# Performance work log

Measured on AMD Instinct MI355X. Metric: run time of the kernel, lower is better.

## Reference

```python
import jax, jax.numpy as jnp
import numpy as np
from jax.ops import segment_sum

NEG_SLOPE = 0.01  # torch F.leaky_relu default

N_NODES = 100000
N_EDGES = 1600000
IN_FEAT = 67
HIDDEN = 256
N_CLASS = 18
N_GRAPHS = 256


def setup_inputs() -> dict:
    key = jax.random.key(0)
    ks = jax.random.split(key, 12)
    h = jax.random.normal(ks[0], (N_NODES, IN_FEAT), dtype=jnp.float32)
    src = jax.random.randint(ks[1], (N_EDGES,), 0, N_NODES, dtype=jnp.int32)
    dst = jax.random.randint(ks[2], (N_EDGES,), 0, N_NODES, dtype=jnp.int32)
    graph_ids = jnp.sort(jax.random.randint(ks[3], (N_NODES,), 0, N_GRAPHS, dtype=jnp.int32))
    s = 0.05
    W1_self = jax.random.normal(ks[4], (IN_FEAT, HIDDEN), dtype=jnp.float32) * s
    W1_neigh = jax.random.normal(ks[5], (IN_FEAT, HIDDEN), dtype=jnp.float32) * s
    b1 = jnp.zeros((HIDDEN,), dtype=jnp.float32)
    W2_self = jax.random.normal(ks[6], (HIDDEN, HIDDEN), dtype=jnp.float32) * s
    W2_neigh = jax.random.normal(ks[7], (HIDDEN, HIDDEN), dtype=jnp.float32) * s
    b2 = jnp.zeros((HIDDEN,), dtype=jnp.float32)
    Wfc = jax.random.normal(ks[8], (HIDDEN, N_CLASS), dtype=jnp.float32) * s
    bfc = jnp.zeros((N_CLASS,), dtype=jnp.float32)
    return {
        "h": h, "W1_self": W1_self, "W1_neigh": W1_neigh, "b1": b1,
        "W2_self": W2_self, "W2_neigh": W2_neigh, "b2": b2,
        "Wfc": Wfc, "bfc": bfc,
        "src": src, "dst": dst, "graph_ids": graph_ids, "num_graphs": N_GRAPHS,
    }


def _sage_mean(h, Wself, Wneigh, b, src, dst, n_nodes):
    # DGL SAGEConv(mean): h_neigh = mean over incoming neighbors; 0 if no neighbors
    agg = segment_sum(h[src], dst, num_segments=n_nodes)          # [N, D]
    deg = segment_sum(jnp.ones_like(dst, dtype=h.dtype), dst, num_segments=n_nodes)
    h_neigh = agg / jnp.maximum(deg, 1.0)[:, None]
    return h @ Wself + h_neigh @ Wneigh + b


def reference(h, W1_self, W1_neigh, b1, W2_self, W2_neigh, b2, Wfc, bfc,
              src, dst, graph_ids, num_graphs):
    n_nodes = h.shape[0]
    x = jax.nn.leaky_relu(_sage_mean(h, W1_self, W1_neigh, b1, src, dst, n_nodes), NEG_SLOPE)
    x = jax.nn.leaky_relu(_sage_mean(x, W2_self, W2_neigh, b2, src, dst, n_nodes), NEG_SLOPE)
    # dgl.mean_nodes: per-graph mean pooling over nodes
    gsum = segment_sum(x, graph_ids, num_segments=num_graphs)       # [G, D]
    gcnt = segment_sum(jnp.ones((n_nodes,), dtype=x.dtype), graph_ids, num_segments=num_graphs)
    hg = gsum / jnp.maximum(gcnt, 1.0)[:, None]
    return hg @ Wfc + bfc  # [G, n_classifier]
```

## Files before the change

kernel.cpp:

```cpp
#include <hip/hip_runtime.h>

#define WAVE 64
#define OW 256
#define LDA1 96
#define NCHUNK 64
#define PBITS 15
#define PBINS (1 << PBITS)
#define NPART 4

typedef short bf16x8 __attribute__((ext_vector_type(8)));
typedef float f32x4  __attribute__((ext_vector_type(4)));
typedef float f32x2  __attribute__((ext_vector_type(2)));

__device__ __forceinline__ unsigned short f2bf(float f) {
    unsigned int u = __float_as_uint(f);
    u = (u + 0x7FFF + ((u >> 16) & 1)) >> 16;
    return (unsigned short)u;
}
__device__ __forceinline__ float bf2f(unsigned short u) {
    return __uint_as_float(((unsigned int)u) << 16);
}
__device__ __forceinline__ float bflo(unsigned int u) { return __uint_as_float(u << 16); }
__device__ __forceinline__ float bfhi(unsigned int u) { return __uint_as_float(u & 0xFFFF0000u); }
__device__ __forceinline__ unsigned int packbf(float lo, float hi) {
    return (unsigned int)f2bf(lo) | ((unsigned int)f2bf(hi) << 16);
}
__device__ __forceinline__ float lrelu(float x) { return x > 0.0f ? x : 0.01f * x; }

__device__ __forceinline__ unsigned int pack4_f8(float v0, float v1, float v2, float v3) {
    int p = __builtin_amdgcn_cvt_pk_fp8_f32(v0, v1, 0, false);
    p = __builtin_amdgcn_cvt_pk_fp8_f32(v2, v3, p, true);
    return (unsigned int)p;
}
__device__ __forceinline__ unsigned char enc1_f8(float v) {
    return (unsigned char)(__builtin_amdgcn_cvt_pk_fp8_f32(v, 0.0f, 0, false) & 0xFF);
}
__device__ __forceinline__ void acc4_f8(float* a, unsigned int u) {
    f32x2 lo = __builtin_amdgcn_cvt_pk_f32_fp8(u, false);
    f32x2 hi = __builtin_amdgcn_cvt_pk_f32_fp8(u, true);
    a[0] += lo.x; a[1] += lo.y; a[2] += hi.x; a[3] += hi.y;
}


__device__ __forceinline__ void pack_b_body(const float* __restrict__ Ws,
                                            const float* __restrict__ Wn,
                                            unsigned short* __restrict__ Bb,
                                            int KHALF, int KT_HALF, int idx) {
    int e  = idx & 7;
    int l  = (idx >> 3) & 63;
    int nt = (idx >> 9) & 15;
    int kt = idx >> 13;
    int n  = nt * 16 + (l & 15);
    int kh = (kt < KT_HALF ? kt : kt - KT_HALF) * 32 + (l >> 4) * 8 + e;
    const float* W = (kt < KT_HALF) ? Ws : Wn;
    float v = (kh < KHALF) ? W[(size_t)kh * OW + n] : 0.0f;
    Bb[idx] = f2bf(v);
}

__global__ void prep_kernel(const float* __restrict__ h, unsigned int* __restrict__ hb,
                            unsigned int* __restrict__ hb8, int N, int K,
                            const float* __restrict__ W1s, const float* __restrict__ W1n,
                            unsigned short* __restrict__ Bb1,
                            const float* __restrict__ W2s, const float* __restrict__ W2n,
                            unsigned short* __restrict__ Bb2) {
    const int tid = blockIdx.x * blockDim.x + threadIdx.x;
    const int nth = gridDim.x * blockDim.x;

    const int tot_h = N * (LDA1 / 2);
    for (int i = tid; i < tot_h; i += nth) {
        int row = i / (LDA1 / 2);
        int c   = (i - row * (LDA1 / 2)) * 2;
        float v0 = (c     < K) ? h[(size_t)row * K + c]     : 0.0f;
        float v1 = (c + 1 < K) ? h[(size_t)row * K + c + 1] : 0.0f;
        hb[i] = packbf(v0, v1);
    }
    const int tot8 = N * (LDA1 / 4);
    for (int i = tid; i < tot8; i += nth) {
        int row = i / (LDA1 / 4);
        int c   = (i - row * (LDA1 / 4)) * 4;
        const float* hr = h + (size_t)row * K;
        float v0 = (c     < K) ? hr[c]     : 0.0f;
        float v1 = (c + 1 < K) ? hr[c + 1] : 0.0f;
        float v2 = (c + 2 < K) ? hr[c + 2] : 0.0f;
        float v3 = (c + 3 < K) ? hr[c + 3] : 0.0f;
        hb8[i] = pack4_f8(v0, v1, v2, v3);
    }
    for (int i = tid; i < 2 * 3 * 16 * 64 * 8; i += nth)
        pack_b_body(W1s, W1n, Bb1, K, 3, i);
    for (int i = tid; i < 2 * 8 * 16 * 64 * 8; i += nth)
        pack_b_body(W2s, W2n, Bb2, OW, 8, i);
}


__global__ __launch_bounds__(512) void hist_kernel(const int* __restrict__ dst, int E, int N,
                                                   unsigned short* __restrict__ hist,
                                                   unsigned short* __restrict__ rank_local) {
    __shared__ unsigned int lcnt[PBINS / 2];
    const int c    = blockIdx.x / NPART;
    const int p    = blockIdx.x - c * NPART;
    const int base = p << PBITS;
    const int nb   = (N - base < PBINS) ? (N - base) : PBINS;
    if (nb <= 0) return;
    const int che = (E + NCHUNK - 1) / NCHUNK;
    const int beg = c * che;
    const int end = (beg + che < E) ? (beg + che) : E;

    for (int i = threadIdx.x; i < PBINS / 2; i += 512) lcnt[i] = 0;
    __syncthreads();

    auto proc = [&](int d, int e) {
        d -= base;
        if ((unsigned)d < (unsigned)nb) {
            unsigned int sh  = (d & 1) * 16;
            unsigned int old = atomicAdd(&lcnt[d >> 1], 1u << sh);
            rank_local[e] = (unsigned short)((old >> sh) & 0xFFFFu);
        }
    };

    if (((beg | end) & 3) == 0) {
        const int4* dst4 = (const int4*)(dst + beg);
        const int n4 = (end - beg) >> 2;
        for (int i = threadIdx.x; i < n4; i += 512) {
            int4 d = dst4[i];
            int e = beg + 4 * i;
            proc(d.x, e + 0);
            proc(d.y, e + 1);
            proc(d.z, e + 2);
            proc(d.w, e + 3);
        }
    } else {
        for (int e = beg + (int)threadIdx.x; e < end; e += 512)
            proc(dst[e], e);
    }
    __syncthreads();

    unsigned short* hrow = hist + (size_t)c * N + base;
    for (int i = threadIdx.x; i < nb; i += 512) {
        unsigned int v = lcnt[i >> 1];
        hrow[i] = (unsigned short)((v >> ((i & 1) * 16)) & 0xFFFFu);
    }
}

__global__ void chunk_scan_kernel(unsigned short* __restrict__ hist, int* __restrict__ cnt,
                                  int N) {
    int bin = blockIdx.x * blockDim.x + threadIdx.x;
    if (bin >= N) return;
    int s = 0;
#pragma unroll 8
    for (int c = 0; c < NCHUNK; ++c) {
        size_t idx = (size_t)c * N + bin;
        int t = hist[idx];
        hist[idx] = (unsigned short)s;
        s += t;
    }
    cnt[bin] = s;
}

__global__ __launch_bounds__(1024) void scan_blocksum(const int* __restrict__ cnt,
                                                      int* __restrict__ bsum, int n) {
    __shared__ int s[1024];
    int i = blockIdx.x * 1024 + threadIdx.x;
    s[threadIdx.x] = (i < n) ? cnt[i] : 0;
    __syncthreads();
    for (int off = 512; off > 0; off >>= 1) {
        if (threadIdx.x < off) s[threadIdx.x] += s[threadIdx.x + off];
        __syncthreads();
    }
    if (threadIdx.x == 0) bsum[blockIdx.x] = s[0];
}

__global__ __launch_bounds__(128) void scan_offsets(int* __restrict__ bsum, int nb) {
    __shared__ int s[128];
    int v = (threadIdx.x < nb) ? bsum[threadIdx.x] : 0;
    s[threadIdx.x] = v;
    __syncthreads();
    for (int off = 1; off < 128; off <<= 1) {
        int t = (threadIdx.x >= off) ? s[threadIdx.x - off] : 0;
        __syncthreads();
        s[threadIdx.x] += t;
        __syncthreads();
    }
    if (threadIdx.x < nb) bsum[threadIdx.x] = s[threadIdx.x] - v;
}

__global__ __launch_bounds__(1024) void scan_write(const int* __restrict__ cnt,
                                                   const int* __restrict__ boff,
                                                   int* __restrict__ rowptr, int n) {
    __shared__ int s[1024];
    int i = blockIdx.x * 1024 + threadIdx.x;
    int v = (i < n) ? cnt[i] : 0;
    s[threadIdx.x] = v;
    __syncthreads();
    for (int off = 1; off < 1024; off <<= 1) {
        int t = (threadIdx.x >= off) ? s[threadIdx.x - off] : 0;
        __syncthreads();
        s[threadIdx.x] += t;
        __syncthreads();
    }
    if (i < n) rowptr[i + 1] = boff[blockIdx.x] + s[threadIdx.x];
    if (i == 0) rowptr[0] = 0;
}

__global__ void fill_kernel(const int* __restrict__ src, const int* __restrict__ dst,
                            const unsigned short* __restrict__ rank_local,
                            const int* __restrict__ rowptr,
                            const unsigned short* __restrict__ hist,
                            int* __restrict__ csr, int E, int N) {
    const int che = (E + NCHUNK - 1) / NCHUNK;
    const int tid = blockIdx.x * blockDim.x + threadIdx.x;
    const int nth = gridDim.x * blockDim.x;

    if ((che & 3) == 0) {
        const int e4 = E >> 2;
        const int4* dst4 = (const int4*)dst;
        const int4* src4 = (const int4*)src;
        const ushort4* r4 = (const ushort4*)rank_local;
        for (int i = tid; i < e4; i += nth) {
            int4 d = dst4[i];
            int4 s = src4[i];
            ushort4 r = r4[i];
            const unsigned short* hrow = hist + (size_t)(4 * i / che) * N;
            csr[rowptr[d.x] + (int)hrow[d.x] + (int)r.x] = s.x;
            csr[rowptr[d.y] + (int)hrow[d.y] + (int)r.y] = s.y;
            csr[rowptr[d.z] + (int)hrow[d.z] + (int)r.z] = s.z;
            csr[rowptr[d.w] + (int)hrow[d.w] + (int)r.w] = s.w;
        }
        for (int e = e4 * 4 + tid; e < E; e += nth) {
            int d = dst[e];
            csr[rowptr[d] + (int)hist[(size_t)(e / che) * N + d] + (int)rank_local[e]] = src[e];
        }
    } else {
        for (int e = tid; e < E; e += nth) {
            int d = dst[e];
            csr[rowptr[d] + (int)hist[(size_t)(e / che) * N + d] + (int)rank_local[e]] = src[e];
        }
    }
}


__global__ void gather_mean256_f8(const unsigned char* __restrict__ feat,
                                  const int* __restrict__ rowptr, const int* __restrict__ csr,
                                  unsigned int* __restrict__ aggm, int N) {
    const int lane = threadIdx.x & (WAVE - 1);
    const int grp  = lane >> 4;
    const int sub  = lane & 15;
    int wave = (blockIdx.x * blockDim.x + threadIdx.x) / WAVE;
    int nw   = (gridDim.x * blockDim.x) / WAVE;

    for (int v = wave; v < N; v += nw) {
        const int beg = rowptr[v], deg = rowptr[v + 1] - beg;
        float a[16];
#pragma unroll
        for (int i = 0; i < 16; ++i) a[i] = 0.0f;

        const int noct = deg >> 3;
        for (int i = 0; i < noct; ++i) {
            int e0 = csr[beg + 8 * i + grp];
            int e1 = csr[beg + 8 * i + 4 + grp];
            uint4 x0 = *(const uint4*)(feat + (size_t)e0 * 256 + sub * 16);
            uint4 x1 = *(const uint4*)(feat + (size_t)e1 * 256 + sub * 16);
            acc4_f8(a + 0,  x0.x); acc4_f8(a + 4,  x0.y);
            acc4_f8(a + 8,  x0.z); acc4_f8(a + 12, x0.w);
            acc4_f8(a + 0,  x1.x); acc4_f8(a + 4,  x1.y);
            acc4_f8(a + 8,  x1.z); acc4_f8(a + 12, x1.w);
        }
        for (int e = (noct << 3) + grp; e < deg; e += 4) {
            int s = csr[beg + e];
            uint4 x = *(const uint4*)(feat + (size_t)s * 256 + sub * 16);
            acc4_f8(a + 0,  x.x); acc4_f8(a + 4,  x.y);
            acc4_f8(a + 8,  x.z); acc4_f8(a + 12, x.w);
        }
#pragma unroll
        for (int i = 0; i < 16; ++i) {
            a[i] += __shfl_xor(a[i], 16);
            a[i] += __shfl_xor(a[i], 32);
        }
        if (grp == 0) {
            float inv = 1.0f / fmaxf((float)deg, 1.0f);
            unsigned int o[8];
#pragma unroll
            for (int i = 0; i < 8; ++i)
                o[i] = packbf(a[2 * i] * inv, a[2 * i + 1] * inv);
            unsigned int* dst0 = aggm + (size_t)v * 128 + sub * 8;
            *(uint4*)(dst0)     = make_uint4(o[0], o[1], o[2], o[3]);
            *(uint4*)(dst0 + 4) = make_uint4(o[4], o[5], o[6], o[7]);
        }
    }
}

__global__ void gather_mean_pad_f8(const unsigned char* __restrict__ feat,
                                   const int* __restrict__ rowptr, const int* __restrict__ csr,
                                   unsigned int* __restrict__ aggm, int N) {
    const int lane = threadIdx.x & (WAVE - 1);
    const int half = lane >> 5;
    const int sub  = lane & 31;
    const bool act = sub < 24;
    int wave = (blockIdx.x * blockDim.x + threadIdx.x) / WAVE;
    int nw   = (gridDim.x * blockDim.x) / WAVE;

    for (int v = wave; v < N; v += nw) {
        const int beg = rowptr[v], deg = rowptr[v + 1] - beg;
        const int npairs = deg >> 1;
        float a[4] = {0.f, 0.f, 0.f, 0.f};

        int p = 0;
        for (; p + 3 < npairs; p += 4) {
            int i0 = csr[beg + 2 * (p + 0) + half];
            int i1 = csr[beg + 2 * (p + 1) + half];
            int i2 = csr[beg + 2 * (p + 2) + half];
            int i3 = csr[beg + 2 * (p + 3) + half];
            if (act) {
                unsigned int x0 = *(const unsigned int*)(feat + (size_t)i0 * 96 + sub * 4);
                unsigned int x1 = *(const unsigned int*)(feat + (size_t)i1 * 96 + sub * 4);
                unsigned int x2 = *(const unsigned int*)(feat + (size_t)i2 * 96 + sub * 4);
                unsigned int x3 = *(const unsigned int*)(feat + (size_t)i3 * 96 + sub * 4);
                acc4_f8(a, x0); acc4_f8(a, x1); acc4_f8(a, x2); acc4_f8(a, x3);
            }
        }
        for (; p < npairs; ++p) {
            int i0 = csr[beg + 2 * p + half];
            if (act) {
                unsigned int x0 = *(const unsigned int*)(feat + (size_t)i0 * 96 + sub * 4);
                acc4_f8(a, x0);
            }
        }
        if ((deg & 1) && half == 0) {
            int i0 = csr[beg + deg - 1];
            if (act) {
                unsigned int x0 = *(const unsigned int*)(feat + (size_t)i0 * 96 + sub * 4);
                acc4_f8(a, x0);
            }
        }
#pragma unroll
        for (int i = 0; i < 4; ++i) a[i] += __shfl_xor(a[i], 32);

        if (half == 0 && act) {
            float inv = 1.0f / fmaxf((float)deg, 1.0f);
            uint2 o;
            o.x = packbf(a[0] * inv, a[1] * inv);
            o.y = packbf(a[2] * inv, a[3] * inv);
            *(uint2*)(aggm + (size_t)v * 48 + sub * 2) = o;
        }
    }
}

template<int KT_HALF, int CHUNK, bool F8OUT>
__global__ __launch_bounds__(256) void sage_mfma(
    const unsigned short* __restrict__ Hs, const unsigned short* __restrict__ Hn, int lda,
    const unsigned short* __restrict__ Bb, const float* __restrict__ bias,
    unsigned short* __restrict__ outb, unsigned char* __restrict__ out8, int M)
{
    constexpr int NT    = 2 * KT_HALF;
    constexpr int NCH   = NT / CHUNK;
    constexpr int CELEM = CHUNK * 16 * 64;
    constexpr int CPT   = CELEM / 256;
    __shared__ bf16x8 Bs[CELEM];

    const int t    = threadIdx.x;
    const int lane = t & 63, wid = t >> 6;
    const int wm   = wid >> 1, wn = wid & 1;
    const int brow = blockIdx.x * 64;
    const int lrow = lane & 15, kblk = lane >> 4;

    const int r0 = brow + wm * 32 + lrow;
    const int r1 = r0 + 16;
    const int r0c = (r0 < M) ? r0 : (M - 1);
    const int r1c = (r1 < M) ? r1 : (M - 1);

    f32x4 acc[2][8];
#pragma unroll
    for (int rt = 0; rt < 2; ++rt)
#pragma unroll
        for (int ct = 0; ct < 8; ++ct) acc[rt][ct] = (f32x4)0.0f;

    auto loadA = [&](int ch, bf16x8 (&a0)[CHUNK], bf16x8 (&a1)[CHUNK]) {
#pragma unroll
        for (int k = 0; k < CHUNK; ++k) {
            int kt = ch * CHUNK + k;
            bool self = kt < KT_HALF;
            int kh = (self ? kt : kt - KT_HALF) * 32 + kblk * 8;
            const unsigned short* srcp = self ? Hs : Hn;
            a0[k] = *(const bf16x8*)(srcp + (size_t)r0c * lda + kh);
            a1[k] = *(const bf16x8*)(srcp + (size_t)r1c * lda + kh);
        }
    };

    const bf16x8* gB = (const bf16x8*)Bb;
    bf16x8 tmpB[CPT];
    bf16x8 a0[CHUNK], a1[CHUNK];
#pragma unroll
    for (int i = 0; i < CPT; ++i) tmpB[i] = gB[i * 256 + t];
    loadA(0, a0, a1);

#pragma unroll
    for (int ch = 0; ch < NCH; ++ch) {
        __syncthreads();
#pragma unroll
        for (int i = 0; i < CPT; ++i) Bs[i * 256 + t] = tmpB[i];
        __syncthreads();

        bf16x8 nB[CPT], n0[CHUNK], n1[CHUNK];
        if (ch + 1 < NCH) {
            const bf16x8* g = gB + (size_t)(ch + 1) * CELEM;
#pragma unroll
            for (int i = 0; i < CPT; ++i) nB[i] = g[i * 256 + t];
            loadA(ch + 1, n0, n1);
        }

#pragma unroll
        for (int k = 0; k < CHUNK; ++k) {
            const bf16x8* bp = &Bs[(k * 16 + wn * 8) * 64 + lane];
#pragma unroll
            for (int ct = 0; ct < 8; ++ct) {
                bf16x8 b = bp[ct * 64];
                acc[0][ct] = __builtin_amdgcn_mfma_f32_16x16x32_bf16(a0[k], b, acc[0][ct], 0, 0, 0);
                acc[1][ct] = __builtin_amdgcn_mfma_f32_16x16x32_bf16(a1[k], b, acc[1][ct], 0, 0, 0);
            }
        }
        if (ch + 1 < NCH) {
#pragma unroll
            for (int i = 0; i < CPT; ++i) tmpB[i] = nB[i];
#pragma unroll
            for (int k = 0; k < CHUNK; ++k) { a0[k] = n0[k]; a1[k] = n1[k]; }
        }
    }

#pragma unroll
    for (int rt = 0; rt < 2; ++rt) {
        int rbase = brow + wm * 32 + rt * 16 + kblk * 4;
#pragma unroll
        for (int ct = 0; ct < 8; ++ct) {
            int col = wn * 128 + ct * 16 + lrow;
            float vb = bias[col];
#pragma unroll
            for (int j = 0; j < 4; ++j) {
                int row = rbase + j;
                if (row < M) {
                    float v = lrelu(acc[rt][ct][j] + vb);
                    outb[(size_t)row * OW + col] = f2bf(v);
                    if (F8OUT)
                        out8[(size_t)row * OW + col] = enc1_f8(v);
                }
            }
        }
    }
}


__global__ __launch_bounds__(256) void pool_fc_kernel(
    const unsigned short* __restrict__ x, const int* __restrict__ gid,
    const float* __restrict__ Wfc, const float* __restrict__ bfc,
    float* __restrict__ out, int N, int C)
{
    int g = blockIdx.x;
    int lo = 0, hi = N;
    while (lo < hi) { int m = (lo + hi) >> 1; if (gid[m] < g) lo = m + 1; else hi = m; }
    int beg = lo;
    hi = N;
    while (lo < hi) { int m = (lo + hi) >> 1; if (gid[m] <= g) lo = m + 1; else hi = m; }
    int end = lo;

    __shared__ float hg[OW];
    int c = threadIdx.x;
    float s0 = 0.f, s1 = 0.f, s2 = 0.f, s3 = 0.f;
    int r = beg;
    for (; r + 3 < end; r += 4) {
        s0 += bf2f(x[(size_t)(r + 0) * OW + c]);
        s1 += bf2f(x[(size_t)(r + 1) * OW + c]);
        s2 += bf2f(x[(size_t)(r + 2) * OW + c]);
        s3 += bf2f(x[(size_t)(r + 3) * OW + c]);
    }
    for (; r < end; ++r) s0 += bf2f(x[(size_t)r * OW + c]);
    float s = (s0 + s1) + (s2 + s3);
    float inv = (end > beg) ? 1.0f / (float)(end - beg) : 0.0f;
    hg[c] = s * inv;
    __syncthreads();

    if (c < C) {
        float a = bfc[c];
        for (int k = 0; k < OW; ++k)
            a = fmaf(hg[k], Wfc[(size_t)k * C + c], a);
        out[(size_t)g * C + c] = a;
    }
}

extern "C" void kernel_launch(void* const* d_in, const int* in_sizes, int n_in,
                              void* d_out, int out_size, void* d_ws, size_t ws_size,
                              hipStream_t stream) {
    const float* h   = (const float*)d_in[0];
    const float* W1s = (const float*)d_in[1];
    const float* W1n = (const float*)d_in[2];
    const float* b1  = (const float*)d_in[3];
    const float* W2s = (const float*)d_in[4];
    const float* W2n = (const float*)d_in[5];
    const float* b2  = (const float*)d_in[6];
    const float* Wfc = (const float*)d_in[7];
    const float* bfc = (const float*)d_in[8];
    const int*   src = (const int*)d_in[9];
    const int*   dst = (const int*)d_in[10];
    const int*   gid = (const int*)d_in[11];

    const int N  = in_sizes[11];
    const int E  = in_sizes[9];
    const int K1 = in_sizes[0] / N;
    const int NC = in_sizes[8];
    const int G  = out_size / NC;

    char* w = (char*)d_ws;
    auto alloc = [&](size_t bytes) { char* p = w; w += (bytes + 255) & ~(size_t)255; return p; };
    unsigned int*   hb     = (unsigned int*)alloc((size_t)N * (LDA1 / 2) * 4);
    unsigned int*   hb8    = (unsigned int*)alloc((size_t)N * LDA1);
    unsigned int*   agg1b  = (unsigned int*)alloc((size_t)N * (LDA1 / 2) * 4);
    unsigned short* x1b    = (unsigned short*)alloc((size_t)N * OW * 2);
    unsigned char*  x1f8   = (unsigned char*)alloc((size_t)N * OW);
    unsigned short* agg2b  = (unsigned short*)alloc((size_t)N * OW * 2);
    int*            rowptr = (int*)alloc((size_t)(N + 1) * 4);
    int*            cnt    = (int*)alloc((size_t)N * 4);
    int*            csr    = (int*)alloc((size_t)E * 4);
    unsigned short* rankl  = (unsigned short*)alloc((size_t)E * 2);
    unsigned short* hist   = (unsigned short*)alloc((size_t)NCHUNK * N * 2);
    int*            bsum   = (int*)alloc(1024 * 4);
    unsigned short* Bb1    = (unsigned short*)alloc((size_t)2 * 3 * 16 * 64 * 8 * 2);
    unsigned short* Bb2    = (unsigned short*)alloc((size_t)2 * 8 * 16 * 64 * 8 * 2);

    float* out = (float*)d_out;
    const int nb = (N + 1023) / 1024;

    hist_kernel<<<NCHUNK * NPART, 512, 0, stream>>>(dst, E, N, hist, rankl);
    chunk_scan_kernel<<<(N + 255) / 256, 256, 0, stream>>>(hist, cnt, N);
    scan_blocksum<<<nb, 1024, 0, stream>>>(cnt, bsum, N);
    scan_offsets<<<1, 128, 0, stream>>>(bsum, nb);
    scan_write<<<nb, 1024, 0, stream>>>(cnt, bsum, rowptr, N);
    fill_kernel<<<2048, 256, 0, stream>>>(src, dst, rankl, rowptr, hist, csr, E, N);

    prep_kernel<<<2048, 256, 0, stream>>>(h, hb, hb8, N, K1, W1s, W1n, Bb1, W2s, W2n, Bb2);

    const int gemm_grid = (N + 63) / 64;

    gather_mean_pad_f8<<<4096, 256, 0, stream>>>((const unsigned char*)hb8, rowptr, csr,
                                                 agg1b, N);
    sage_mfma<3, 2, true><<<gemm_grid, 256, 0, stream>>>((const unsigned short*)hb,
                                                         (const unsigned short*)agg1b, LDA1,
                                                         Bb1, b1, x1b, x1f8, N);

    gather_mean256_f8<<<4096, 256, 0, stream>>>(x1f8, rowptr, csr,
                                                (unsigned int*)agg2b, N);
    sage_mfma<8, 2, false><<<gemm_grid, 256, 0, stream>>>(x1b, agg2b, OW, Bb2, b2,
                                                          x1b, nullptr, N);

    pool_fc_kernel<<<G, 256, 0, stream>>>(x1b, gid, Wfc, bfc, out, N, NC);
}
```

Before: 355.1 us.

## Merge histogram with input prep kernel and fuse chunk scan with block sums

The histogram kernel and the feature/weight packing kernel become one launch, with separate block ranges running the two independent jobs concurrently. The per-bin chunk scan now also does the per-block reduction that the separate scan_blocksum kernel used to do. This removes two kernel launches and lets the latency-bound histogram overlap with the bandwidth-bound prep. The cost is that prep blocks now also reserve the histogram's 64KB of shared memory, which lowers occupancy, and the chunk scan runs at 1024 threads per block.

After: 357.6 us. About the same (+0.7%).

```diff
diff --git a/kernel.cpp b/kernel.cpp
--- a/kernel.cpp
+++ b/kernel.cpp
@@ -7,6 +7,7 @@
 #define PBITS 15
 #define PBINS (1 << PBITS)
 #define NPART 4
+#define PREPB 512
 
 typedef short bf16x8 __attribute__((ext_vector_type(8)));
 typedef float f32x4  __attribute__((ext_vector_type(4)));
@@ -57,110 +58,111 @@
     Bb[idx] = f2bf(v);
 }
 
-__global__ void prep_kernel(const float* __restrict__ h, unsigned int* __restrict__ hb,
-                            unsigned int* __restrict__ hb8, int N, int K,
-                            const float* __restrict__ W1s, const float* __restrict__ W1n,
-                            unsigned short* __restrict__ Bb1,
-                            const float* __restrict__ W2s, const float* __restrict__ W2n,
-                            unsigned short* __restrict__ Bb2) {
-    const int tid = blockIdx.x * blockDim.x + threadIdx.x;
-    const int nth = gridDim.x * blockDim.x;
-
-    const int tot_h = N * (LDA1 / 2);
-    for (int i = tid; i < tot_h; i += nth) {
-        int row = i / (LDA1 / 2);
-        int c   = (i - row * (LDA1 / 2)) * 2;
-        float v0 = (c     < K) ? h[(size_t)row * K + c]     : 0.0f;
-        float v1 = (c + 1 < K) ? h[(size_t)row * K + c + 1] : 0.0f;
-        hb[i] = packbf(v0, v1);
-    }
-    const int tot8 = N * (LDA1 / 4);
-    for (int i = tid; i < tot8; i += nth) {
-        int row = i / (LDA1 / 4);
-        int c   = (i - row * (LDA1 / 4)) * 4;
-        const float* hr = h + (size_t)row * K;
-        float v0 = (c     < K) ? hr[c]     : 0.0f;
-        float v1 = (c + 1 < K) ? hr[c + 1] : 0.0f;
-        float v2 = (c + 2 < K) ? hr[c + 2] : 0.0f;
-        float v3 = (c + 3 < K) ? hr[c + 3] : 0.0f;
-        hb8[i] = pack4_f8(v0, v1, v2, v3);
-    }
-    for (int i = tid; i < 2 * 3 * 16 * 64 * 8; i += nth)
-        pack_b_body(W1s, W1n, Bb1, K, 3, i);
-    for (int i = tid; i < 2 * 8 * 16 * 64 * 8; i += nth)
-        pack_b_body(W2s, W2n, Bb2, OW, 8, i);
-}
-
-
-__global__ __launch_bounds__(512) void hist_kernel(const int* __restrict__ dst, int E, int N,
-                                                   unsigned short* __restrict__ hist,
-                                                   unsigned short* __restrict__ rank_local) {
+__global__ __launch_bounds__(512) void hist_prep_kernel(
+    const int* __restrict__ dst, int E, int N,
+    unsigned short* __restrict__ hist, unsigned short* __restrict__ rank_local,
+    const float* __restrict__ h, unsigned int* __restrict__ hb,
+    unsigned int* __restrict__ hb8, int K,
+    const float* __restrict__ W1s, const float* __restrict__ W1n,
+    unsigned short* __restrict__ Bb1,
+    const float* __restrict__ W2s, const float* __restrict__ W2n,
+    unsigned short* __restrict__ Bb2)
+{
     __shared__ unsigned int lcnt[PBINS / 2];
-    const int c    = blockIdx.x / NPART;
-    const int p    = blockIdx.x - c * NPART;
-    const int base = p << PBITS;
-    const int nb   = (N - base < PBINS) ? (N - base) : PBINS;
-    if (nb <= 0) return;
-    const int che = (E + NCHUNK - 1) / NCHUNK;
-    const int beg = c * che;
-    const int end = (beg + che < E) ? (beg + che) : E;
-
-    for (int i = threadIdx.x; i < PBINS / 2; i += 512) lcnt[i] = 0;
-    __syncthreads();
-
-    auto proc = [&](int d, int e) {
-        d -= base;
-        if ((unsigned)d < (unsigned)nb) {
-            unsigned int sh  = (d & 1) * 16;
-            unsigned int old = atomicAdd(&lcnt[d >> 1], 1u << sh);
-            rank_local[e] = (unsigned short)((old >> sh) & 0xFFFFu);
-        }
-    };
-
-    if (((beg | end) & 3) == 0) {
-        const int4* dst4 = (const int4*)(dst + beg);
-        const int n4 = (end - beg) >> 2;
-        for (int i = threadIdx.x; i < n4; i += 512) {
-            int4 d = dst4[i];
-            int e = beg + 4 * i;
-            proc(d.x, e + 0);
-            proc(d.y, e + 1);
-            proc(d.z, e + 2);
-            proc(d.w, e + 3);
+    const int HB = NCHUNK * NPART;
+
+    if (blockIdx.x < HB) {
+        const int c    = blockIdx.x / NPART;
+        const int p    = blockIdx.x - c * NPART;
+        const int base = p << PBITS;
+        const int nb   = (N - base < PBINS) ? (N - base) : PBINS;
+        if (nb <= 0) return;
+        const int che = (E + NCHUNK - 1) / NCHUNK;
+        const int beg = c * che;
+        const int end = (beg + che < E) ? (beg + che) : E;
+
+        for (int i = threadIdx.x; i < PBINS / 2; i += 512) lcnt[i] = 0;
+        __syncthreads();
+
+        auto proc = [&](int d, int e) {
+            d -= base;
+            if ((unsigned)d < (unsigned)nb) {
+                unsigned int sh  = (d & 1) * 16;
+                unsigned int old = atomicAdd(&lcnt[d >> 1], 1u << sh);
+                rank_local[e] = (unsigned short)((old >> sh) & 0xFFFFu);
+            }
+        };
+
+        if (((beg | end) & 3) == 0) {
+            const int4* dst4 = (const int4*)(dst + beg);
+            const int n4 = (end - beg) >> 2;
+            for (int i = threadIdx.x; i < n4; i += 512) {
+                int4 d = dst4[i];
+                int e = beg + 4 * i;
+                proc(d.x, e + 0);
+                proc(d.y, e + 1);
+                proc(d.z, e + 2);
+                proc(d.w, e + 3);
+            }
+        } else {
+            for (int e = beg + (int)threadIdx.x; e < end; e += 512)
+                proc(dst[e], e);
+        }
+        __syncthreads();
+
+        unsigned short* hrow = hist + (size_t)c * N + base;
+        for (int i = threadIdx.x; i < nb; i += 512) {
+            unsigned int v = lcnt[i >> 1];
+            hrow[i] = (unsigned short)((v >> ((i & 1) * 16)) & 0xFFFFu);
         }
     } else {
-        for (int e = beg + (int)threadIdx.x; e < end; e += 512)
-            proc(dst[e], e);
-    }
-    __syncthreads();
-
-    unsigned short* hrow = hist + (size_t)c * N + base;
-    for (int i = threadIdx.x; i < nb; i += 512) {
-        unsigned int v = lcnt[i >> 1];
-        hrow[i] = (unsigned short)((v >> ((i & 1) * 16)) & 0xFFFFu);
-    }
-}
-
-__global__ void chunk_scan_kernel(unsigned short* __restrict__ hist, int* __restrict__ cnt,
-                                  int N) {
-    int bin = blockIdx.x * blockDim.x + threadIdx.x;
-    if (bin >= N) return;
-    int s = 0;
+        const int tid = (blockIdx.x - HB) * 512 + threadIdx.x;
+        const int nth = PREPB * 512;
+
+        const int tot_h = N * (LDA1 / 2);
+        for (int i = tid; i < tot_h; i += nth) {
+            int row = i / (LDA1 / 2);
+            int c   = (i - row * (LDA1 / 2)) * 2;
+            float v0 = (c     < K) ? h[(size_t)row * K + c]     : 0.0f;
+            float v1 = (c + 1 < K) ? h[(size_t)row * K + c + 1] : 0.0f;
+            hb[i] = packbf(v0, v1);
+        }
+        const int tot8 = N * (LDA1 / 4);
+        for (int i = tid; i < tot8; i += nth) {
+            int row = i / (LDA1 / 4);
+            int c   = (i - row * (LDA1 / 4)) * 4;
+            const float* hr = h + (size_t)row * K;
+            float v0 = (c     < K) ? hr[c]     : 0.0f;
+            float v1 = (c + 1 < K) ? hr[c + 1] : 0.0f;
+            float v2 = (c + 2 < K) ? hr[c + 2] : 0.0f;
+            float v3 = (c + 3 < K) ? hr[c + 3] : 0.0f;
+            hb8[i] = pack4_f8(v0, v1, v2, v3);
+        }
+        for (int i = tid; i < 2 * 3 * 16 * 64 * 8; i += nth)
+            pack_b_body(W1s, W1n, Bb1, K, 3, i);
+        for (int i = tid; i < 2 * 8 * 16 * 64 * 8; i += nth)
+            pack_b_body(W2s, W2n, Bb2, OW, 8, i);
+    }
+}
+
+
+__global__ __launch_bounds__(1024) void chunk_scan_kernel(unsigned short* __restrict__ hist,
+                                                          int* __restrict__ cnt,
+                                                          int* __restrict__ bsum, int N) {
+    __shared__ int s[1024];
+    int bin = blockIdx.x * 1024 + threadIdx.x;
+    int total = 0;
+    if (bin < N) {
 #pragma unroll 8
-    for (int c = 0; c < NCHUNK; ++c) {
-        size_t idx = (size_t)c * N + bin;
-        int t = hist[idx];
-        hist[idx] = (unsigned short)s;
-        s += t;
-    }
-    cnt[bin] = s;
-}
-
-__global__ __launch_bounds__(1024) void scan_blocksum(const int* __restrict__ cnt,
-                                                      int* __restrict__ bsum, int n) {
-    __shared__ int s[1024];
-    int i = blockIdx.x * 1024 + threadIdx.x;
-    s[threadIdx.x] = (i < n) ? cnt[i] : 0;
+        for (int c = 0; c < NCHUNK; ++c) {
+            size_t idx = (size_t)c * N + bin;
+            int t = hist[idx];
+            hist[idx] = (unsigned short)total;
+            total += t;
+        }
+        cnt[bin] = total;
+    }
+    s[threadIdx.x] = total;
     __syncthreads();
     for (int off = 512; off > 0; off >>= 1) {
         if (threadIdx.x < off) s[threadIdx.x] += s[threadIdx.x + off];
@@ -526,14 +528,13 @@
     float* out = (float*)d_out;
     const int nb = (N + 1023) / 1024;
 
-    hist_kernel<<<NCHUNK * NPART, 512, 0, stream>>>(dst, E, N, hist, rankl);
-    chunk_scan_kernel<<<(N + 255) / 256, 256, 0, stream>>>(hist, cnt, N);
-    scan_blocksum<<<nb, 1024, 0, stream>>>(cnt, bsum, N);
+    hist_prep_kernel<<<NCHUNK * NPART + PREPB, 512, 0, stream>>>(
+        dst, E, N, hist, rankl, h, hb, hb8, K1, W1s, W1n, Bb1, W2s, W2n, Bb2);
+
+    chunk_scan_kernel<<<nb, 1024, 0, stream>>>(hist, cnt, bsum, N);
     scan_offsets<<<1, 128, 0, stream>>>(bsum, nb);
     scan_write<<<nb, 1024, 0, stream>>>(cnt, bsum, rowptr, N);
     fill_kernel<<<2048, 256, 0, stream>>>(src, dst, rankl, rowptr, hist, csr, E, N);
-
-    prep_kernel<<<2048, 256, 0, stream>>>(h, hb, hb8, N, K1, W1s, W1n, Bb1, W2s, W2n, Bb2);
 
     const int gemm_grid = (N + 63) / 64;
 
```
